# Kernel tuning notes

Hardware: AMD Instinct MI355X
Metric: run time of the kernel (lower is better)

The kernel has to match this reference:

```python
import jax, jax.numpy as jnp
import numpy as np
import math

C_S, C_Z = 384, 128
N_HEAD, C = 12, 16
N_QP, N_PV = 4, 8
B, N_RES = 1, 384


def quat_to_rot(q):
    # q: (..., 4) unnormalized quaternion -> (..., 3, 3) rotation matrix
    q = q / jnp.linalg.norm(q, axis=-1, keepdims=True)
    w, x, y, z = q[..., 0], q[..., 1], q[..., 2], q[..., 3]
    R = jnp.stack([
        1 - 2 * (y * y + z * z), 2 * (x * y - w * z), 2 * (x * z + w * y),
        2 * (x * y + w * z), 1 - 2 * (x * x + z * z), 2 * (y * z - w * x),
        2 * (x * z - w * y), 2 * (y * z + w * x), 1 - 2 * (x * x + y * y),
    ], axis=-1)
    return R.reshape(q.shape[:-1] + (3, 3))


def warp_3d_point(T, p):
    # T: (..., 1, 1, N, 4, 4) rigid transforms; p: (..., H, P, N, 3)
    R = T[..., :3, :3]
    t = T[..., :3, 3]
    return jnp.squeeze(R @ p[..., None], -1) + t


def warp_3d_point_inv(T, p):
    # Inverse rigid transform: R^T (p - t)
    R = T[..., :3, :3]
    t = T[..., :3, 3]
    return jnp.squeeze(jnp.swapaxes(R, -1, -2) @ (p - t)[..., None], -1)


def setup_inputs() -> dict:
    key = jax.random.key(0)
    ks = jax.random.split(key, 24)
    s = jax.random.normal(ks[0], (B, N_RES, C_S), dtype=jnp.float32)
    z = jax.random.normal(ks[1], (B, N_RES, N_RES, C_Z), dtype=jnp.float32)
    # Build rigid backbone transforms T (rotation from random quaternion + translation)
    quat = jax.random.normal(ks[2], (B, N_RES, 4), dtype=jnp.float32)
    trans = jax.random.normal(ks[3], (B, N_RES, 3), dtype=jnp.float32) * 10.0
    R = quat_to_rot(quat)
    T = jnp.zeros((B, N_RES, 4, 4), dtype=jnp.float32)
    T = T.at[..., :3, :3].set(R)
    T = T.at[..., :3, 3].set(trans)
    T = T.at[..., 3, 3].set(1.0)

    def lin(k, din, dout):
        kw, kb = jax.random.split(k)
        W = jax.random.normal(kw, (din, dout), dtype=jnp.float32) * 0.02
        b = jax.random.normal(kb, (dout,), dtype=jnp.float32) * 0.01
        return W, b

    Wq, bq = lin(ks[4], C_S, N_HEAD * C)
    Wk, bk = lin(ks[5], C_S, N_HEAD * C)
    Wv, bv = lin(ks[6], C_S, N_HEAD * C)
    Wqp, bqp = lin(ks[7], C_S, 3 * N_QP * N_HEAD)
    Wkp, bkp = lin(ks[8], C_S, 3 * N_QP * N_HEAD)
    Wvp, bvp = lin(ks[9], C_S, 3 * N_PV * N_HEAD)
    Wb, bb = lin(ks[10], C_Z, N_HEAD)
    d_out_in = N_HEAD * C_Z + N_HEAD * C + N_HEAD * 4 * N_PV
    Wo, bo = lin(ks[11], d_out_in, C_S)
    head_weights = jax.random.normal(ks[12], (N_HEAD,), dtype=jnp.float32) * 0.1
    return dict(s=s, z=z, T=T, Wq=Wq, bq=bq, Wk=Wk, bk=bk, Wv=Wv, bv=bv,
                Wqp=Wqp, bqp=bqp, Wkp=Wkp, bkp=bkp, Wvp=Wvp, bvp=bvp,
                Wb=Wb, bb=bb, Wo=Wo, bo=bo, head_weights=head_weights)


def ipa_forward(s, z, T, Wq, bq, Wk, bk, Wv, bv, Wqp, bqp, Wkp, bkp,
                Wvp, bvp, Wb, bb, Wo, bo, head_weights):
    batch = s.shape[:-2]
    n = s.shape[-2]
    # --- prepare qkv ---
    def heads(x):  # (..., N, H*C) -> (..., H, N, C)
        return jnp.moveaxis(x.reshape(batch + (n, N_HEAD, C)), -3, -2)
    q = heads(s @ Wq + bq)
    k = heads(s @ Wk + bk)
    v = heads(s @ Wv + bv)

    def pts(x, P):  # (..., N, 3*H*P) -> (..., H, P, N, 3)
        x = x.reshape(batch + (n, 3, N_HEAD, P))
        return jnp.moveaxis(x, (-4, -3), (-2, -1))
    qp = pts(s @ Wqp + bqp, N_QP)
    kp = pts(s @ Wkp + bkp, N_QP)
    vp = pts(s @ Wvp + bvp, N_PV)

    # --- attention scores (Alg 22 line 7) ---
    wc = math.sqrt(2.0 / (9.0 * N_QP))
    wl = math.sqrt(1.0 / 3.0)
    gamma = jax.nn.softplus(head_weights).reshape(-1, 1, 1)  # (H,1,1)
    q = q * (1.0 / math.sqrt(C))
    bias = jnp.moveaxis(z @ Wb + bb, -1, -3)  # (..., H, N, N)
    qk = jnp.einsum('...hic,...hjc->...hij', q, k)
    T_bc = T.reshape(batch + (1, 1, n, 4, 4))
    tqp = warp_3d_point(T_bc, qp)[..., :, None, :]   # (..., H, QP, N, 1, 3)
    tkp = warp_3d_point(T_bc, kp)[..., None, :, :]   # (..., H, QP, 1, N, 3)
    sq_dist = jnp.sum((tqp - tkp) ** 2, axis=-1)      # (..., H, QP, N, N)
    qpkp_term = gamma * (wc / 2.0) * jnp.sum(sq_dist, axis=-3)  # (..., H, N, N)
    att = jax.nn.softmax(wl * (qk + bias - qpkp_term), axis=-1)

    # --- outputs ---
    pairwise = jnp.einsum('...ijc,...hij->...hic', z, att)
    pairwise = jnp.moveaxis(pairwise, -3, -2).reshape(batch + (n, N_HEAD * C_Z))
    v_out = jnp.einsum('...hij,...hjc->...hic', att, v)
    v_out = jnp.moveaxis(v_out, -3, -2).reshape(batch + (n, N_HEAD * C))
    vt = warp_3d_point(T_bc, vp)                                # (..., H, PV, N, 3)
    v_att = jnp.einsum('...hij,...hkjp->...hkip', att, vt)     # (..., H, PV, N, 3)
    v_tr = warp_3d_point_inv(T_bc, v_att)                       # (..., H, PV, N, 3)
    v_tr = jnp.einsum('...hpic->...ichp', v_tr)                 # (..., N, 3, H, PV)
    norm = jnp.linalg.norm(v_tr, axis=-3, keepdims=True)        # (..., N, 1, H, PV)
    vp_norm = norm.reshape(batch + (n, N_HEAD * N_PV))
    vp_out = v_tr.reshape(batch + (n, 3 * N_HEAD * N_PV))

    out = jnp.concatenate([v_out, vp_out, vp_norm, pairwise], axis=-1)
    return out @ Wo + bo


def reference(s, z, T, Wq, bq, Wk, bk, Wv, bv, Wqp, bqp, Wkp, bkp,
              Wvp, bvp, Wb, bb, Wo, bo, head_weights):
    return ipa_forward(s, z, T, Wq, bq, Wk, bk, Wv, bv, Wqp, bqp, Wkp, bkp,
                       Wvp, bvp, Wb, bb, Wo, bo, head_weights)
```

## Files before the change

### kernel.cpp

```cpp
#include <hip/hip_runtime.h>
#include <math.h>

#define NRES 384
#define NH   12
#define WLc 0.5773502691896258f
#define WCc 0.23570226039551587f

typedef __attribute__((ext_vector_type(8))) _Float16 half8;
typedef __attribute__((ext_vector_type(4))) float f32x4;

#define OFF_P    0
#define OFF_PW   0
#define OFF_SH   442368
#define OFF_WCT  516096
#define OFF_BCT  737280
#define OFF_QE   738432
#define OFF_KE   885888
#define OFF_VET  1033344
#define OFF_WOT  1143936
#define OFF_CAT  1549440
#define OFF_ATT  1660032
#define OFF_BIAS 2544768

__global__ __launch_bounds__(256) void pack_bias(
    const float* __restrict__ s,  const float* __restrict__ z,
    const float* __restrict__ Wq,  const float* __restrict__ bq,
    const float* __restrict__ Wk,  const float* __restrict__ bk,
    const float* __restrict__ Wv,  const float* __restrict__ bv,
    const float* __restrict__ Wqp, const float* __restrict__ bqp,
    const float* __restrict__ Wkp, const float* __restrict__ bkp,
    const float* __restrict__ Wvp, const float* __restrict__ bvp,
    const float* __restrict__ Wb,  const float* __restrict__ bb,
    const float* __restrict__ Wo,
    float* __restrict__ ws)
{
    int b = blockIdx.x, t = threadIdx.x;
    __shared__ float tile[64 * 65];
    __shared__ _Float16 wbT[16 * 136];
    __shared__ float sbb[16];

    if (b >= 451) {
        _Float16* biasb = (_Float16*)(ws + OFF_BIAS);
        int bi = b - 451;
        size_t m0 = (size_t)bi * 64;
        if (t < 128) {
            #pragma unroll
            for (int h = 0; h < 12; h++) wbT[h * 136 + t] = (_Float16)(WLc * Wb[t * 12 + h]);
            #pragma unroll
            for (int h = 12; h < 16; h++) wbT[h * 136 + t] = (_Float16)0.f;
        }
        if (t < 16) sbb[t] = (t < 12) ? WLc * bb[t] : 0.f;
        __syncthreads();
        int w = t >> 6, lane = t & 63;
        int m = lane & 15, q = lane >> 4;
        size_t ri = m0 + w * 16 + m;
        const float* zr = z + ri * 128 + q * 8;
        f32x4 acc = {0};
        #pragma unroll
        for (int sI = 0; sI < 4; sI++) {
            float4 v0 = *(const float4*)(zr + sI * 32);
            float4 v1 = *(const float4*)(zr + sI * 32 + 4);
            half8 a;
            a[0]=(_Float16)v0.x; a[1]=(_Float16)v0.y; a[2]=(_Float16)v0.z; a[3]=(_Float16)v0.w;
            a[4]=(_Float16)v1.x; a[5]=(_Float16)v1.y; a[6]=(_Float16)v1.z; a[7]=(_Float16)v1.w;
            half8 bf = *(const half8*)(wbT + m * 136 + sI * 32 + q * 8);
            acc = __builtin_amdgcn_mfma_f32_16x16x32_f16(a, bf, acc, 0, 0, 0);
        }
        if (m < 12) {
            #pragma unroll
            for (int r = 0; r < 4; r++)
                biasb[(size_t)m * 147456 + m0 + w * 16 + q * 4 + r] = (_Float16)(acc[r] + sbb[m]);
        }
        return;
    }

    _Float16* sh  = (_Float16*)(ws + OFF_SH);
    _Float16* wct = (_Float16*)(ws + OFF_WCT);
    _Float16* wot = (_Float16*)(ws + OFF_WOT);
    float* bct = ws + OFF_BCT;

    if (b < 144) {
        int id = b * 256 + t;
        float4 v = ((const float4*)s)[id];
        _Float16 r[4] = { (_Float16)v.x, (_Float16)v.y, (_Float16)v.z, (_Float16)v.w };
        *(uint2*)(sh + id * 4) = *(uint2*)r;
        return;
    }
    if (b < 252) {
        int ti = b - 144;
        int k0 = (ti % 6) * 64, n0 = (ti / 6) * 64;
        int cl = t & 63, rg = t >> 6;
        int ncat = n0 + cl;
        const float* W; int dout, col;
        if      (ncat < 192) { W = Wq;  dout = 192; col = ncat; }
        else if (ncat < 384) { W = Wk;  dout = 192; col = ncat - 192; }
        else if (ncat < 576) { W = Wv;  dout = 192; col = ncat - 384; }
        else if (ncat < 720) { W = Wqp; dout = 144; col = ncat - 576; }
        else if (ncat < 864) { W = Wkp; dout = 144; col = ncat - 720; }
        else                 { W = Wvp; dout = 288; col = ncat - 864; }
        #pragma unroll
        for (int u = 0; u < 16; u++) {
            int r = rg * 16 + u;
            tile[r * 65 + cl] = W[(size_t)(k0 + r) * dout + col];
        }
        __syncthreads();
        #pragma unroll
        for (int u2 = 0; u2 < 2; u2++) {
            int item = t + 256 * u2;
            int nl = item >> 3, kg = item & 7;
            half8 rr;
            #pragma unroll
            for (int jj = 0; jj < 8; jj++) rr[jj] = (_Float16)tile[(kg * 8 + jj) * 65 + nl];
            *(half8*)(wct + (size_t)(n0 + nl) * 384 + k0 + kg * 8) = rr;
        }
        return;
    }
    if (b < 450) {
        int ti = b - 252;
        int k0 = (ti % 33) * 64, n0 = (ti / 33) * 64;
        int cl = t & 63, rg = t >> 6;
        #pragma unroll
        for (int u = 0; u < 16; u++) {
            int r = rg * 16 + u;
            tile[r * 65 + cl] = Wo[(size_t)(k0 + r) * 384 + n0 + cl];
        }
        __syncthreads();
        #pragma unroll
        for (int u2 = 0; u2 < 2; u2++) {
            int item = t + 256 * u2;
            int nl = item >> 3, kg = item & 7;
            half8 rr;
            #pragma unroll
            for (int jj = 0; jj < 8; jj++) rr[jj] = (_Float16)tile[(kg * 8 + jj) * 65 + nl];
            *(half8*)(wot + (size_t)(n0 + nl) * 2112 + k0 + kg * 8) = rr;
        }
        return;
    }
    for (int e = t; e < 1152; e += 256) {
        float bv_;
        if      (e < 192) bv_ = bq[e];
        else if (e < 384) bv_ = bk[e - 192];
        else if (e < 576) bv_ = bv[e - 384];
        else if (e < 720) bv_ = bqp[e - 576];
        else if (e < 864) bv_ = bkp[e - 720];
        else              bv_ = bvp[e - 864];
        bct[e] = bv_;
    }
}

__global__ __launch_bounds__(128) void proj_mfma(float* __restrict__ ws)
{
    const _Float16* sh  = (const _Float16*)(ws + OFF_SH);
    const _Float16* wct = (const _Float16*)(ws + OFF_WCT);
    const float* bct = ws + OFF_BCT;
    float* P = ws + OFF_P;

    int t = threadIdx.x, w = t >> 6, lane = t & 63;
    int m = lane & 15, q = lane >> 4;
    int n0 = blockIdx.x * 64, m0 = blockIdx.y * 32 + w * 16;

    f32x4 acc[4] = {0};
    const _Float16* arow = sh + (size_t)(m0 + m) * 384;
    #pragma unroll 4
    for (int s = 0; s < 12; s++) {
        int k = s * 32 + q * 8;
        half8 a = *(const half8*)(arow + k);
        #pragma unroll
        for (int nt = 0; nt < 4; nt++) {
            half8 b = *(const half8*)(wct + (size_t)(n0 + nt * 16 + m) * 384 + k);
            acc[nt] = __builtin_amdgcn_mfma_f32_16x16x32_f16(a, b, acc[nt], 0, 0, 0);
        }
    }
    #pragma unroll
    for (int nt = 0; nt < 4; nt++) {
        int col = n0 + nt * 16 + m;
        float bias = bct[col];
        #pragma unroll
        for (int r = 0; r < 4; r++)
            P[(size_t)(m0 + q * 4 + r) * 1152 + col] = acc[nt][r] + bias;
    }
}

__global__ __launch_bounds__(192) void prep_kernel(
    const float* __restrict__ T, const float* __restrict__ hw,
    float* __restrict__ ws)
{
    int i = blockIdx.x, t = threadIdx.x;
    const float* pr = ws + OFF_P + (size_t)i * 1152;
    float* Qe = ws + OFF_QE;
    float* Ke = ws + OFF_KE;
    _Float16* vet = (_Float16*)(ws + OFF_VET);

    __shared__ float sT[16], sG[12];
    __shared__ float sTQ[12][4][3], sTK[12][4][3];
    if (t < 16) sT[t] = T[i * 16 + t];
    if (t < 12) { float x = hw[t]; sG[t] = (x > 20.f) ? x : log1pf(__expf(x)); }
    __syncthreads();
    float R00=sT[0],R01=sT[1],R02=sT[2],t0=sT[3];
    float R10=sT[4],R11=sT[5],R12=sT[6],t1=sT[7];
    float R20=sT[8],R21=sT[9],R22=sT[10],t2=sT[11];

    if (t < 48) {
        int h = t >> 2, p = t & 3;
        float a0 = pr[576 + 0*48 + h*4 + p], a1 = pr[576 + 1*48 + h*4 + p], a2 = pr[576 + 2*48 + h*4 + p];
        sTQ[h][p][0] = R00*a0 + R01*a1 + R02*a2 + t0;
        sTQ[h][p][1] = R10*a0 + R11*a1 + R12*a2 + t1;
        sTQ[h][p][2] = R20*a0 + R21*a1 + R22*a2 + t2;
    } else if (t < 96) {
        int tt = t - 48, h = tt >> 2, p = tt & 3;
        float a0 = pr[720 + 0*48 + h*4 + p], a1 = pr[720 + 1*48 + h*4 + p], a2 = pr[720 + 2*48 + h*4 + p];
        sTK[h][p][0] = R00*a0 + R01*a1 + R02*a2 + t0;
        sTK[h][p][1] = R10*a0 + R11*a1 + R12*a2 + t1;
        sTK[h][p][2] = R20*a0 + R21*a1 + R22*a2 + t2;
    } else {
        int tt = t - 96, h = tt >> 3, p = tt & 7;
        float a0 = pr[864 + 0*96 + h*8 + p], a1 = pr[864 + 1*96 + h*8 + p], a2 = pr[864 + 2*96 + h*8 + p];
        vet[(size_t)(h*48 + 16 + p*3 + 0) * 384 + i] = (_Float16)(R00*a0 + R01*a1 + R02*a2 + t0);
        vet[(size_t)(h*48 + 16 + p*3 + 1) * 384 + i] = (_Float16)(R10*a0 + R11*a1 + R12*a2 + t1);
        vet[(size_t)(h*48 + 16 + p*3 + 2) * 384 + i] = (_Float16)(R20*a0 + R21*a1 + R22*a2 + t2);
    }
    {
        int h = t >> 4, c = t & 15;
        vet[(size_t)(h*48 + c) * 384 + i] = (_Float16)pr[384 + h*16 + c];
        if (t < 96) vet[(size_t)((t>>3)*48 + 40 + (t&7)) * 384 + i] = (_Float16)0.f;
        Qe[(size_t)i*384 + h*32 + c] = WLc * 0.25f * pr[h*16 + c];
        Ke[((size_t)h*384 + i)*32 + c] = pr[192 + h*16 + c];
    }
    __syncthreads();
    if (t < 144) {
        int h = t / 12, d = t % 12, p = d / 3, r = d % 3;
        float gw = WLc * sG[h] * WCc;
        Qe[(size_t)i*384 + h*32 + 16 + d] = gw * sTQ[h][p][r];
        Ke[((size_t)h*384 + i)*32 + 16 + d] = sTK[h][p][r];
    }
    if (t < 12) {
        int h = t;
        float sqq = 0.f, sqk = 0.f;
        #pragma unroll
        for (int p = 0; p < 4; p++)
            #pragma unroll
            for (int r = 0; r < 3; r++) { sqq += sTQ[h][p][r]*sTQ[h][p][r]; sqk += sTK[h][p][r]*sTK[h][p][r]; }
        float gw = WLc * sG[h] * WCc;
        Qe[(size_t)i*384 + h*32 + 28] = -0.5f * gw;
        Qe[(size_t)i*384 + h*32 + 29] = -0.5f * gw * sqq;
        Qe[(size_t)i*384 + h*32 + 30] = 0.f;
        Qe[(size_t)i*384 + h*32 + 31] = 0.f;
        Ke[((size_t)h*384 + i)*32 + 28] = sqk;
        Ke[((size_t)h*384 + i)*32 + 29] = 1.f;
        Ke[((size_t)h*384 + i)*32 + 30] = 0.f;
        Ke[((size_t)h*384 + i)*32 + 31] = 0.f;
    }
}

__global__ __launch_bounds__(512) void logits_out40(
    const float* __restrict__ T, const float* __restrict__ bo,
    float* __restrict__ ws, float* __restrict__ out)
{
    __shared__ float sQe[8 * 32];
    __shared__ float sLg[8][384];
    __shared__ float sMS[16];
    __shared__ _Float16 sAttL[8 * 392];
    __shared__ float sO[8 * 49];
    __shared__ float sT8[8 * 16];

    int h = blockIdx.y, i0 = blockIdx.x * 8;
    int t = threadIdx.x;
    const float* Qe = ws + OFF_QE;
    const float* Ke = ws + OFF_KE;
    const _Float16* biasb = (const _Float16*)(ws + OFF_BIAS);
    const _Float16* vet = (const _Float16*)(ws + OFF_VET);
    _Float16* attg = (_Float16*)(ws + OFF_ATT);
    _Float16* catb = (_Float16*)(ws + OFF_CAT);

    {
        int bid = blockIdx.y * 48 + blockIdx.x;
        if (t < 256) {
            int e = bid * 256 + t;
            out[e] = bo[e % 384];
            ((float4*)(ws + OFF_PW))[e] = (float4){0.f, 0.f, 0.f, 0.f};
        }
    }
    if (t < 256)
        sQe[t] = Qe[(size_t)(i0 + (t >> 5)) * 384 + h * 32 + (t & 31)];
    if (t < 128)
        sT8[t] = T[(size_t)(i0 + (t >> 4)) * 16 + (t & 15)];
    __syncthreads();

    float lgv[8];
    if (t < 384) {
        int j = t;
        float ke[32];
        const float4* kr = (const float4*)(Ke + ((size_t)h * 384 + j) * 32);
        #pragma unroll
        for (int u = 0; u < 8; u++) { float4 v = kr[u]; ke[u*4]=v.x; ke[u*4+1]=v.y; ke[u*4+2]=v.z; ke[u*4+3]=v.w; }
        #pragma unroll
        for (int ii = 0; ii < 8; ii++) {
            float acc = (float)biasb[(size_t)h * 147456 + (size_t)(i0 + ii) * 384 + j];
            #pragma unroll
            for (int c = 0; c < 32; c++) acc += sQe[ii * 32 + c] * ke[c];
            lgv[ii] = acc;
            sLg[ii][j] = acc;
        }
    }
    __syncthreads();
    {
        int w = t >> 6, lane = t & 63;
        float vv[6], mx = -1e30f;
        #pragma unroll
        for (int u = 0; u < 6; u++) { vv[u] = sLg[w][lane + 64 * u]; mx = fmaxf(mx, vv[u]); }
        #pragma unroll
        for (int off = 1; off < 64; off <<= 1) mx = fmaxf(mx, __shfl_xor(mx, off));
        float sm = 0.f;
        #pragma unroll
        for (int u = 0; u < 6; u++) sm += __expf(vv[u] - mx);
        #pragma unroll
        for (int off = 1; off < 64; off <<= 1) sm += __shfl_xor(sm, off);
        if (lane == 0) { sMS[w] = mx; sMS[8 + w] = sm; }
    }
    __syncthreads();
    if (t < 384) {
        int j = t;
        #pragma unroll
        for (int ii = 0; ii < 8; ii++) {
            float a = __expf(lgv[ii] - sMS[ii]) * (1.0f / sMS[8 + ii]);
            attg[((size_t)h * 384 + i0 + ii) * 384 + j] = (_Float16)a;
            sAttL[ii * 392 + j] = (_Float16)a;
        }
    }
    __syncthreads();

    int w = t >> 6, lane = t & 63;
    int m16 = lane & 15, q = lane >> 4;
    if (w < 3) {
        int nt = w;
        f32x4 acc = {0};
        #pragma unroll 3
        for (int s = 0; s < 12; s++) {
            int k = s * 32 + q * 8;
            half8 a;
            if (m16 < 8) a = *(const half8*)(sAttL + m16 * 392 + k);
            else         a = (half8){0,0,0,0,0,0,0,0};
            half8 bfr = *(const half8*)(vet + (size_t)(h * 48 + nt * 16 + m16) * 384 + k);
            acc = __builtin_amdgcn_mfma_f32_16x16x32_f16(a, bfr, acc, 0, 0, 0);
        }
        #pragma unroll
        for (int r = 0; r < 4; r++) {
            int row = q * 4 + r;
            if (row < 8) sO[row * 49 + nt * 16 + m16] = acc[r];
        }
    }
    __syncthreads();

    if (t < 128) {
        int il = t >> 4, c = t & 15;
        catb[(size_t)(i0 + il) * 576 + h * 16 + c] = (_Float16)sO[il * 49 + c];
    }
    if (t < 64) {
        int il = t >> 3, p = t & 7;
        const float* o = sO + il * 49 + 16 + p * 3;
        const float* Ti = sT8 + il * 16;
        float x0 = o[0] - Ti[3], x1 = o[1] - Ti[7], x2 = o[2] - Ti[11];
        float r0 = Ti[0]*x0 + Ti[4]*x1 + Ti[8]*x2;
        float r1 = Ti[1]*x0 + Ti[5]*x1 + Ti[9]*x2;
        float r2 = Ti[2]*x0 + Ti[6]*x1 + Ti[10]*x2;
        _Float16* cr = catb + (size_t)(i0 + il) * 576;
        cr[192 + 0*96 + h*8 + p] = (_Float16)r0;
        cr[192 + 1*96 + h*8 + p] = (_Float16)r1;
        cr[192 + 2*96 + h*8 + p] = (_Float16)r2;
        cr[480 + h*8 + p] = (_Float16)sqrtf(r0*r0 + r1*r1 + r2*r2);
    }
}

__global__ __launch_bounds__(256) void pairwise_mfma(
    const float* __restrict__ z, float* __restrict__ ws)
{
    __shared__ _Float16 ztT[128 * 136];
    int i = blockIdx.x, jc = blockIdx.y, j0 = jc * 128;
    int t = threadIdx.x, w = t >> 6, lane = t & 63;
    int m16 = lane & 15, q = lane >> 4;
    const _Float16* attg = (const _Float16*)(ws + OFF_ATT);
    float* PW = ws + OFF_PW;

    {
        int c = t & 127, jg = t >> 7;
        const float* zbase = z + ((size_t)i * 384 + j0 + jg * 8) * 128 + c;
        #pragma unroll
        for (int jt = 0; jt < 8; jt++) {
            half8 r;
            #pragma unroll
            for (int u = 0; u < 8; u++)
                r[u] = (_Float16)zbase[(size_t)(jt * 16 + u) * 128];
            *(half8*)(ztT + c * 136 + jt * 16 + jg * 8) = r;
        }
    }
    __syncthreads();

    f32x4 acc0 = {0}, acc1 = {0};
    const _Float16* arow = attg + ((size_t)(m16 < 12 ? m16 : 0) * 384 + i) * 384 + j0;
    #pragma unroll
    for (int ks = 0; ks < 4; ks++) {
        int k = ks * 32 + q * 8;
        half8 a;
        if (m16 < 12) a = *(const half8*)(arow + k);
        else          a = (half8){0,0,0,0,0,0,0,0};
        half8 b0 = *(const half8*)(ztT + (w * 32 + m16) * 136 + k);
        half8 b1 = *(const half8*)(ztT + (w * 32 + 16 + m16) * 136 + k);
        acc0 = __builtin_amdgcn_mfma_f32_16x16x32_f16(a, b0, acc0, 0, 0, 0);
        acc1 = __builtin_amdgcn_mfma_f32_16x16x32_f16(a, b1, acc1, 0, 0, 0);
    }
    if (q < 3) {
        #pragma unroll
        for (int r = 0; r < 4; r++) {
            int h = q * 4 + r;
            atomicAdd(&PW[(size_t)i * 1536 + h * 128 + w * 32 + m16],      acc0[r]);
            atomicAdd(&PW[(size_t)i * 1536 + h * 128 + w * 32 + 16 + m16], acc1[r]);
        }
    }
}

__global__ __launch_bounds__(128) void outgemm_mfma(float* __restrict__ ws, float* __restrict__ out)
{
    const _Float16* catb = (const _Float16*)(ws + OFF_CAT);
    const float* PW = ws + OFF_PW;
    const _Float16* wot = (const _Float16*)(ws + OFF_WOT);

    int t = threadIdx.x, w = t >> 6, lane = t & 63;
    int m = lane & 15, q = lane >> 4;
    int n0 = blockIdx.x * 64;
    int m0 = blockIdx.y * 32 + w * 16;
    int kbase = blockIdx.z * 352;

    f32x4 acc[4] = {0};
    int row = m0 + m;
    #pragma unroll 2
    for (int s = 0; s < 11; s++) {
        int kb = kbase + s * 32;
        int k = kb + q * 8;
        half8 a;
        if (kb < 576) {
            a = *(const half8*)(catb + (size_t)row * 576 + k);
        } else {
            const float* pwp = PW + (size_t)row * 1536 + (k - 576);
            float4 u0 = ((const float4*)pwp)[0];
            float4 u1 = ((const float4*)pwp)[1];
            a[0]=(_Float16)u0.x; a[1]=(_Float16)u0.y; a[2]=(_Float16)u0.z; a[3]=(_Float16)u0.w;
            a[4]=(_Float16)u1.x; a[5]=(_Float16)u1.y; a[6]=(_Float16)u1.z; a[7]=(_Float16)u1.w;
        }
        #pragma unroll
        for (int nt = 0; nt < 4; nt++) {
            half8 b = *(const half8*)(wot + (size_t)(n0 + nt * 16 + m) * 2112 + k);
            acc[nt] = __builtin_amdgcn_mfma_f32_16x16x32_f16(a, b, acc[nt], 0, 0, 0);
        }
    }
    #pragma unroll
    for (int nt = 0; nt < 4; nt++) {
        int col = n0 + nt * 16 + m;
        #pragma unroll
        for (int r = 0; r < 4; r++)
            atomicAdd(&out[(size_t)(m0 + q * 4 + r) * 384 + col], acc[nt][r]);
    }
}

extern "C" void kernel_launch(void* const* d_in, const int* in_sizes, int n_in,
                              void* d_out, int out_size, void* d_ws, size_t ws_size,
                              hipStream_t stream)
{
    const float* s   = (const float*)d_in[0];
    const float* z   = (const float*)d_in[1];
    const float* T   = (const float*)d_in[2];
    const float* Wq  = (const float*)d_in[3];
    const float* bq  = (const float*)d_in[4];
    const float* Wk  = (const float*)d_in[5];
    const float* bk  = (const float*)d_in[6];
    const float* Wv  = (const float*)d_in[7];
    const float* bv  = (const float*)d_in[8];
    const float* Wqp = (const float*)d_in[9];
    const float* bqp = (const float*)d_in[10];
    const float* Wkp = (const float*)d_in[11];
    const float* bkp = (const float*)d_in[12];
    const float* Wvp = (const float*)d_in[13];
    const float* bvp = (const float*)d_in[14];
    const float* Wb  = (const float*)d_in[15];
    const float* bb  = (const float*)d_in[16];
    const float* Wo  = (const float*)d_in[17];
    const float* bo  = (const float*)d_in[18];
    const float* hw  = (const float*)d_in[19];
    float* ws  = (float*)d_ws;
    float* out = (float*)d_out;

    pack_bias<<<2755, 256, 0, stream>>>(s, z, Wq, bq, Wk, bk, Wv, bv,
                                        Wqp, bqp, Wkp, bkp, Wvp, bvp, Wb, bb, Wo, ws);
    proj_mfma<<<dim3(18, 12), 128, 0, stream>>>(ws);
    prep_kernel<<<384, 192, 0, stream>>>(T, hw, ws);
    logits_out40<<<dim3(48, 12), 512, 0, stream>>>(T, bo, ws, out);
    pairwise_mfma<<<dim3(384, 3), 256, 0, stream>>>(z, ws);
    outgemm_mfma<<<dim3(6, 12, 6), 128, 0, stream>>>(ws, out);
}
```

Before: 209.2 us.

## Remove atomics: fuse pairwise result into fp16 concat buffer and split-K in-block

New measurement: 215.0 us. +2.8%, slower.

```diff
diff --git a/kernel.cpp b/kernel.cpp
--- a/kernel.cpp
+++ b/kernel.cpp
@@ -7,10 +7,10 @@
 #define WCc 0.23570226039551587f
 
 typedef __attribute__((ext_vector_type(8))) _Float16 half8;
+typedef __attribute__((ext_vector_type(2))) _Float16 half2v;
 typedef __attribute__((ext_vector_type(4))) float f32x4;
 
 #define OFF_P    0
-#define OFF_PW   0
 #define OFF_SH   442368
 #define OFF_WCT  516096
 #define OFF_BCT  737280
@@ -19,8 +19,8 @@
 #define OFF_VET  1033344
 #define OFF_WOT  1143936
 #define OFF_CAT  1549440
-#define OFF_ATT  1660032
-#define OFF_BIAS 2544768
+#define OFF_ATT  1954944
+#define OFF_BIAS 2839680
 
 __global__ __launch_bounds__(256) void pack_bias(
     const float* __restrict__ s,  const float* __restrict__ z,
@@ -148,36 +148,50 @@
     }
 }
 
-__global__ __launch_bounds__(128) void proj_mfma(float* __restrict__ ws)
+__global__ __launch_bounds__(256) void proj_mfma(float* __restrict__ ws)
 {
     const _Float16* sh  = (const _Float16*)(ws + OFF_SH);
     const _Float16* wct = (const _Float16*)(ws + OFF_WCT);
     const float* bct = ws + OFF_BCT;
     float* P = ws + OFF_P;
 
+    __shared__ float sAcc[2][16][65];
+
     int t = threadIdx.x, w = t >> 6, lane = t & 63;
     int m = lane & 15, q = lane >> 4;
-    int n0 = blockIdx.x * 64, m0 = blockIdx.y * 32 + w * 16;
+    int mh = w & 1, kh = w >> 1;
+    int n0 = blockIdx.x * 64, m0 = blockIdx.y * 32 + mh * 16;
 
     f32x4 acc[4] = {0};
-    const _Float16* arow = sh + (size_t)(m0 + m) * 384;
-    #pragma unroll 4
-    for (int s = 0; s < 12; s++) {
+    const _Float16* arow = sh + (size_t)(m0 + m) * 384 + kh * 192;
+    #pragma unroll 3
+    for (int s = 0; s < 6; s++) {
         int k = s * 32 + q * 8;
         half8 a = *(const half8*)(arow + k);
         #pragma unroll
         for (int nt = 0; nt < 4; nt++) {
-            half8 b = *(const half8*)(wct + (size_t)(n0 + nt * 16 + m) * 384 + k);
+            half8 b = *(const half8*)(wct + (size_t)(n0 + nt * 16 + m) * 384 + kh * 192 + k);
             acc[nt] = __builtin_amdgcn_mfma_f32_16x16x32_f16(a, b, acc[nt], 0, 0, 0);
         }
     }
-    #pragma unroll
-    for (int nt = 0; nt < 4; nt++) {
-        int col = n0 + nt * 16 + m;
-        float bias = bct[col];
-        #pragma unroll
-        for (int r = 0; r < 4; r++)
-            P[(size_t)(m0 + q * 4 + r) * 1152 + col] = acc[nt][r] + bias;
+    if (kh == 0) {
+        #pragma unroll
+        for (int nt = 0; nt < 4; nt++)
+            #pragma unroll
+            for (int r = 0; r < 4; r++)
+                sAcc[mh][q * 4 + r][nt * 16 + m] = acc[nt][r];
+    }
+    __syncthreads();
+    if (kh == 1) {
+        #pragma unroll
+        for (int nt = 0; nt < 4; nt++) {
+            int col = n0 + nt * 16 + m;
+            float bias = bct[col];
+            #pragma unroll
+            for (int r = 0; r < 4; r++)
+                P[(size_t)(m0 + q * 4 + r) * 1152 + col] =
+                    acc[nt][r] + sAcc[mh][q * 4 + r][nt * 16 + m] + bias;
+        }
     }
 }
 
@@ -253,8 +267,7 @@
 }
 
 __global__ __launch_bounds__(512) void logits_out40(
-    const float* __restrict__ T, const float* __restrict__ bo,
-    float* __restrict__ ws, float* __restrict__ out)
+    const float* __restrict__ T, float* __restrict__ ws)
 {
     __shared__ float sQe[8 * 32];
     __shared__ float sLg[8][384];
@@ -272,14 +285,6 @@
     _Float16* attg = (_Float16*)(ws + OFF_ATT);
     _Float16* catb = (_Float16*)(ws + OFF_CAT);
 
-    {
-        int bid = blockIdx.y * 48 + blockIdx.x;
-        if (t < 256) {
-            int e = bid * 256 + t;
-            out[e] = bo[e % 384];
-            ((float4*)(ws + OFF_PW))[e] = (float4){0.f, 0.f, 0.f, 0.f};
-        }
-    }
     if (t < 256)
         sQe[t] = Qe[(size_t)(i0 + (t >> 5)) * 384 + h * 32 + (t & 31)];
     if (t < 128)
@@ -353,7 +358,7 @@
 
     if (t < 128) {
         int il = t >> 4, c = t & 15;
-        catb[(size_t)(i0 + il) * 576 + h * 16 + c] = (_Float16)sO[il * 49 + c];
+        catb[(size_t)(i0 + il) * 2112 + h * 16 + c] = (_Float16)sO[il * 49 + c];
     }
     if (t < 64) {
         int il = t >> 3, p = t & 7;
@@ -363,7 +368,7 @@
         float r0 = Ti[0]*x0 + Ti[4]*x1 + Ti[8]*x2;
         float r1 = Ti[1]*x0 + Ti[5]*x1 + Ti[9]*x2;
         float r2 = Ti[2]*x0 + Ti[6]*x1 + Ti[10]*x2;
-        _Float16* cr = catb + (size_t)(i0 + il) * 576;
+        _Float16* cr = catb + (size_t)(i0 + il) * 2112;
         cr[192 + 0*96 + h*8 + p] = (_Float16)r0;
         cr[192 + 1*96 + h*8 + p] = (_Float16)r1;
         cr[192 + 2*96 + h*8 + p] = (_Float16)r2;
@@ -375,89 +380,105 @@
     const float* __restrict__ z, float* __restrict__ ws)
 {
     __shared__ _Float16 ztT[128 * 136];
-    int i = blockIdx.x, jc = blockIdx.y, j0 = jc * 128;
+    __shared__ __attribute__((aligned(16))) _Float16 sPW[1536];
+    int i = blockIdx.x;
     int t = threadIdx.x, w = t >> 6, lane = t & 63;
     int m16 = lane & 15, q = lane >> 4;
     const _Float16* attg = (const _Float16*)(ws + OFF_ATT);
-    float* PW = ws + OFF_PW;
-
-    {
-        int c = t & 127, jg = t >> 7;
-        const float* zbase = z + ((size_t)i * 384 + j0 + jg * 8) * 128 + c;
-        #pragma unroll
-        for (int jt = 0; jt < 8; jt++) {
-            half8 r;
-            #pragma unroll
-            for (int u = 0; u < 8; u++)
-                r[u] = (_Float16)zbase[(size_t)(jt * 16 + u) * 128];
-            *(half8*)(ztT + c * 136 + jt * 16 + jg * 8) = r;
-        }
-    }
-    __syncthreads();
+    _Float16* catb = (_Float16*)(ws + OFF_CAT);
 
     f32x4 acc0 = {0}, acc1 = {0};
-    const _Float16* arow = attg + ((size_t)(m16 < 12 ? m16 : 0) * 384 + i) * 384 + j0;
-    #pragma unroll
-    for (int ks = 0; ks < 4; ks++) {
-        int k = ks * 32 + q * 8;
-        half8 a;
-        if (m16 < 12) a = *(const half8*)(arow + k);
-        else          a = (half8){0,0,0,0,0,0,0,0};
-        half8 b0 = *(const half8*)(ztT + (w * 32 + m16) * 136 + k);
-        half8 b1 = *(const half8*)(ztT + (w * 32 + 16 + m16) * 136 + k);
-        acc0 = __builtin_amdgcn_mfma_f32_16x16x32_f16(a, b0, acc0, 0, 0, 0);
-        acc1 = __builtin_amdgcn_mfma_f32_16x16x32_f16(a, b1, acc1, 0, 0, 0);
+    const _Float16* arow = attg + ((size_t)(m16 < 12 ? m16 : 0) * 384 + i) * 384;
+
+    int cq = t & 31, g = t >> 5;
+    for (int jc = 0; jc < 3; jc++) {
+        if (jc) __syncthreads();
+        const float* zb = z + ((size_t)i * 384 + jc * 128) * 128;
+        #pragma unroll
+        for (int jp = 0; jp < 8; jp++) {
+            int j = g * 16 + jp * 2;
+            float4 v0 = *(const float4*)(zb + (size_t)j * 128 + cq * 4);
+            float4 v1 = *(const float4*)(zb + (size_t)(j + 1) * 128 + cq * 4);
+            half2v c0 = {(_Float16)v0.x, (_Float16)v1.x};
+            half2v c1 = {(_Float16)v0.y, (_Float16)v1.y};
+            half2v c2 = {(_Float16)v0.z, (_Float16)v1.z};
+            half2v c3 = {(_Float16)v0.w, (_Float16)v1.w};
+            *(half2v*)(ztT + (cq * 4 + 0) * 136 + j) = c0;
+            *(half2v*)(ztT + (cq * 4 + 1) * 136 + j) = c1;
+            *(half2v*)(ztT + (cq * 4 + 2) * 136 + j) = c2;
+            *(half2v*)(ztT + (cq * 4 + 3) * 136 + j) = c3;
+        }
+        __syncthreads();
+        #pragma unroll
+        for (int ks = 0; ks < 4; ks++) {
+            int k = ks * 32 + q * 8;
+            half8 a;
+            if (m16 < 12) a = *(const half8*)(arow + jc * 128 + k);
+            else          a = (half8){0,0,0,0,0,0,0,0};
+            half8 b0 = *(const half8*)(ztT + (w * 32 + m16) * 136 + k);
+            half8 b1 = *(const half8*)(ztT + (w * 32 + 16 + m16) * 136 + k);
+            acc0 = __builtin_amdgcn_mfma_f32_16x16x32_f16(a, b0, acc0, 0, 0, 0);
+            acc1 = __builtin_amdgcn_mfma_f32_16x16x32_f16(a, b1, acc1, 0, 0, 0);
+        }
     }
     if (q < 3) {
         #pragma unroll
         for (int r = 0; r < 4; r++) {
             int h = q * 4 + r;
-            atomicAdd(&PW[(size_t)i * 1536 + h * 128 + w * 32 + m16],      acc0[r]);
-            atomicAdd(&PW[(size_t)i * 1536 + h * 128 + w * 32 + 16 + m16], acc1[r]);
-        }
-    }
-}
-
-__global__ __launch_bounds__(128) void outgemm_mfma(float* __restrict__ ws, float* __restrict__ out)
+            sPW[h * 128 + w * 32 + m16]      = (_Float16)acc0[r];
+            sPW[h * 128 + w * 32 + 16 + m16] = (_Float16)acc1[r];
+        }
+    }
+    __syncthreads();
+    if (t < 192)
+        *(half8*)(catb + (size_t)i * 2112 + 576 + t * 8) = *(const half8*)(sPW + t * 8);
+}
+
+__global__ __launch_bounds__(256) void outgemm_mfma(
+    float* __restrict__ ws, const float* __restrict__ bo, float* __restrict__ out)
 {
     const _Float16* catb = (const _Float16*)(ws + OFF_CAT);
-    const float* PW = ws + OFF_PW;
     const _Float16* wot = (const _Float16*)(ws + OFF_WOT);
+
+    __shared__ float sAcc[2][16][65];
 
     int t = threadIdx.x, w = t >> 6, lane = t & 63;
     int m = lane & 15, q = lane >> 4;
+    int mh = w & 1, kh = w >> 1;
     int n0 = blockIdx.x * 64;
-    int m0 = blockIdx.y * 32 + w * 16;
-    int kbase = blockIdx.z * 352;
+    int m0 = blockIdx.y * 32 + mh * 16;
 
     f32x4 acc[4] = {0};
     int row = m0 + m;
-    #pragma unroll 2
-    for (int s = 0; s < 11; s++) {
-        int kb = kbase + s * 32;
-        int k = kb + q * 8;
-        half8 a;
-        if (kb < 576) {
-            a = *(const half8*)(catb + (size_t)row * 576 + k);
-        } else {
-            const float* pwp = PW + (size_t)row * 1536 + (k - 576);
-            float4 u0 = ((const float4*)pwp)[0];
-            float4 u1 = ((const float4*)pwp)[1];
-            a[0]=(_Float16)u0.x; a[1]=(_Float16)u0.y; a[2]=(_Float16)u0.z; a[3]=(_Float16)u0.w;
-            a[4]=(_Float16)u1.x; a[5]=(_Float16)u1.y; a[6]=(_Float16)u1.z; a[7]=(_Float16)u1.w;
-        }
+    const _Float16* ar = catb + (size_t)row * 2112 + kh * 1056;
+    #pragma unroll 3
+    for (int s = 0; s < 33; s++) {
+        int k = s * 32 + q * 8;
+        half8 a = *(const half8*)(ar + k);
         #pragma unroll
         for (int nt = 0; nt < 4; nt++) {
-            half8 b = *(const half8*)(wot + (size_t)(n0 + nt * 16 + m) * 2112 + k);
+            half8 b = *(const half8*)(wot + (size_t)(n0 + nt * 16 + m) * 2112 + kh * 1056 + k);
             acc[nt] = __builtin_amdgcn_mfma_f32_16x16x32_f16(a, b, acc[nt], 0, 0, 0);
         }
     }
-    #pragma unroll
-    for (int nt = 0; nt < 4; nt++) {
-        int col = n0 + nt * 16 + m;
-        #pragma unroll
-        for (int r = 0; r < 4; r++)
-            atomicAdd(&out[(size_t)(m0 + q * 4 + r) * 384 + col], acc[nt][r]);
+    if (kh == 0) {
+        #pragma unroll
+        for (int nt = 0; nt < 4; nt++)
+            #pragma unroll
+            for (int r = 0; r < 4; r++)
+                sAcc[mh][q * 4 + r][nt * 16 + m] = acc[nt][r];
+    }
+    __syncthreads();
+    if (kh == 1) {
+        #pragma unroll
+        for (int nt = 0; nt < 4; nt++) {
+            int col = n0 + nt * 16 + m;
+            float bv = bo[col];
+            #pragma unroll
+            for (int r = 0; r < 4; r++)
+                out[(size_t)(m0 + q * 4 + r) * 384 + col] =
+                    acc[nt][r] + sAcc[mh][q * 4 + r][nt * 16 + m] + bv;
+        }
     }
 }
 
@@ -490,9 +511,9 @@
 
     pack_bias<<<2755, 256, 0, stream>>>(s, z, Wq, bq, Wk, bk, Wv, bv,
                                         Wqp, bqp, Wkp, bkp, Wvp, bvp, Wb, bb, Wo, ws);
-    proj_mfma<<<dim3(18, 12), 128, 0, stream>>>(ws);
+    proj_mfma<<<dim3(18, 12), 256, 0, stream>>>(ws);
     prep_kernel<<<384, 192, 0, stream>>>(T, hw, ws);
-    logits_out40<<<dim3(48, 12), 512, 0, stream>>>(T, bo, ws, out);
-    pairwise_mfma<<<dim3(384, 3), 256, 0, stream>>>(z, ws);
-    outgemm_mfma<<<dim3(6, 12, 6), 128, 0, stream>>>(ws, out);
-}
+    logits_out40<<<dim3(48, 12), 512, 0, stream>>>(T, ws);
+    pairwise_mfma<<<384, 256, 0, stream>>>(z, ws);
+    outgemm_mfma<<<dim3(6, 12), 256, 0, stream>>>(ws, bo, out);
+}
```
